# Kernel tuning notes

Measured on AMD Instinct MI355X. Metric: run time of the kernel, lower is better.

The kernel has to match this reference:

```python
import jax, jax.numpy as jnp
import numpy as np

B, S, P, J = 32, 128, 2, 17
DIN, DOUT, DRNN, DHID = 2, 3, 128, 256
N = P * J
DT = 0.1   # delta_t from init
K = 4      # Euler steps, hardcoded k=int(4) in source


def setup_inputs() -> dict:
    key = jax.random.key(0)
    ks = jax.random.split(key, 12)
    g = lambda k, sh, fan: (jax.random.normal(k, sh, jnp.float32) / np.sqrt(fan)).astype(jnp.float32)
    d = {}
    d['x2d'] = jax.random.normal(ks[0], (B, S, P, J, DIN), jnp.float32)
    d['mask'] = jax.random.randint(ks[1], (B, S, P, J, 1), 0, 2).astype(jnp.int32)
    # ODE MLP: DRNN -> DHID -> DHID -> DRNN (num_hidden=2 hidden layers, tanh)
    d['ode_w0'] = g(ks[2], (DRNN, DHID), DRNN); d['ode_b0'] = jnp.zeros((DHID,), jnp.float32)
    d['ode_w1'] = g(ks[3], (DHID, DHID), DHID); d['ode_b1'] = jnp.zeros((DHID,), jnp.float32)
    d['ode_w2'] = g(ks[4], (DHID, DRNN), DHID); d['ode_b2'] = jnp.zeros((DRNN,), jnp.float32)
    # GRU cell 0: input DIN -> hidden DRNN ; GRU cell 1: input DRNN -> hidden DRNN
    d['wih0'] = g(ks[5], (DIN, 3 * DRNN), DIN);  d['whh0'] = g(ks[6], (DRNN, 3 * DRNN), DRNN)
    d['bih0'] = jnp.zeros((3 * DRNN,), jnp.float32); d['bhh0'] = jnp.zeros((3 * DRNN,), jnp.float32)
    d['wih1'] = g(ks[7], (DRNN, 3 * DRNN), DRNN); d['whh1'] = g(ks[8], (DRNN, 3 * DRNN), DRNN)
    d['bih1'] = jnp.zeros((3 * DRNN,), jnp.float32); d['bhh1'] = jnp.zeros((3 * DRNN,), jnp.float32)
    d['wout'] = g(ks[9], (DRNN, DOUT), DRNN); d['bout'] = jnp.zeros((DOUT,), jnp.float32)
    d['h0'] = 0.01 * jax.random.normal(ks[10], (1, 1, DRNN), jnp.float32)
    return d


def _ode(h, w0, b0, w1, b1, w2, b2):
    h = jnp.tanh(h @ w0 + b0)
    h = jnp.tanh(h @ w1 + b1)
    return h @ w2 + b2


def _gru(x, h, wih, whh, bih, bhh):
    gi = x @ wih + bih
    gh = h @ whh + bhh
    ir, iz, ig = jnp.split(gi, 3, axis=-1)
    hr, hz, hg = jnp.split(gh, 3, axis=-1)
    r = jax.nn.sigmoid(ir + hr)
    z = jax.nn.sigmoid(iz + hz)
    n = jnp.tanh(ig + r * hg)
    return (1.0 - z) * n + z * h


def reference(x2d, mask, ode_w0, ode_b0, ode_w1, ode_b1, ode_w2, ode_b2,
              wih0, whh0, bih0, bhh0, wih1, whh1, bih1, bhh1, wout, bout, h0):
    m = mask.astype(x2d.dtype)                      # (B,S,P,J,1)
    xs = (x2d * m).reshape(B, S, N, DIN)            # masked 2D input
    ms = m.reshape(B, S, N, 1)
    h_init = jnp.broadcast_to(h0, (B, N, DRNN))

    def step(h, inp):
        x, mm = inp                                 # (B,N,DIN), (B,N,1)
        h1 = h
        for _ in range(K):                          # 4 Euler ODE steps
            h1 = h1 + DT * _ode(h1, ode_w0, ode_b0, ode_w1, ode_b1, ode_w2, ode_b2)
        h2 = _gru(x, h1, wih0, whh0, bih0, bhh0)    # stacked GRU, both conditioned on h1
        h2 = _gru(h2, h1, wih1, whh1, bih1, bhh1)
        h_next = h1 * (1.0 - mm) + h2 * mm
        return h_next, h1

    _, hs = jax.lax.scan(step, h_init,
                         (jnp.swapaxes(xs, 0, 1), jnp.swapaxes(ms, 0, 1)))
    hs = jnp.swapaxes(hs, 0, 1)                     # (B,S,N,DRNN)
    ys = (hs @ wout + bout).reshape(B, S, P, J, DOUT)
    return ys
```

## Files before the change

### kernel.cpp

```cpp
#include <hip/hip_runtime.h>

typedef _Float16 f16x8 __attribute__((ext_vector_type(8)));
typedef float f32x4 __attribute__((ext_vector_type(4)));

constexpr int S_ = 128;
constexpr float DT_ = 0.1f;
constexpr float LS = 2048.0f;
constexpr float INV = 1.0f / 2048.0f;

#define MFMA(a, b, c) __builtin_amdgcn_mfma_f32_16x16x32_f16((a), (b), (c), 0, 0, 0)

#define OB0   0
#define OB1   256
#define OB2   512
#define OBHH0 640
#define OBIH0 1024
#define OBIH1 1408
#define OBHH1 1792
#define NBIAS 2176

__device__ __forceinline__ float fast_tanh(float x) {
    float e = __expf(2.0f * x);
    return 1.0f - 2.0f / (e + 1.0f);
}
__device__ __forceinline__ float fast_sigmoid(float x) {
    return 1.0f / (1.0f + __expf(-x));
}

__global__ void prep_hl(const float* __restrict__ src, _Float16* __restrict__ hi,
                        _Float16* __restrict__ lo, int K, int N) {
    int e = blockIdx.x * 256 + threadIdx.x;
    if (e >= K * N) return;
    int tile = e >> 9, r = e & 511;
    int lane = r >> 3, j = r & 7;
    int KT = K >> 5;
    int nt = tile / KT, kt = tile - nt * KT;
    int k = kt * 32 + ((lane >> 4) << 3) + j;
    int n = nt * 16 + (lane & 15);
    float v = src[k * N + n];
    _Float16 h = (_Float16)v;
    hi[e] = h;
    lo[e] = (_Float16)((v - (float)h) * LS);
}

__global__ __launch_bounds__(512) void odernn_mfma(
    const float* __restrict__ x2d, const int* __restrict__ maskp,
    const _Float16* __restrict__ w0h, const _Float16* __restrict__ w0l,
    const _Float16* __restrict__ w1hg, const _Float16* __restrict__ w1lg,
    const _Float16* __restrict__ w2h, const _Float16* __restrict__ w2l,
    const _Float16* __restrict__ hh0h, const _Float16* __restrict__ hh0l,
    const _Float16* __restrict__ ih1h, const _Float16* __restrict__ ih1l,
    const _Float16* __restrict__ hh1h, const _Float16* __restrict__ hh1l,
    const float* __restrict__ b0, const float* __restrict__ b1,
    const float* __restrict__ b2, const float* __restrict__ bhh0,
    const float* __restrict__ bih0, const float* __restrict__ wih0,
    const float* __restrict__ bih1, const float* __restrict__ bhh1,
    const float* __restrict__ wout, const float* __restrict__ bout,
    const float* __restrict__ h0, float* __restrict__ out)
{
    __shared__ float hF[16][128];
    __shared__ _Float16 bAh[16][264], bAl[16][264];
    __shared__ _Float16 bBh[16][264], bBl[16][264];
    __shared__ _Float16 bHh[16][136], bHl[16][136];
    __shared__ float sbias[NBIAS];
    __shared__ float swi0[768];
    __shared__ float swout[384];
    __shared__ float sbout[4];
    __shared__ float sx0[16], sx1[16], smm[16];
    __shared__ int sIdx[16];

    const int tid = (int)threadIdx.x;
    const int wv = tid >> 6;
    const int l = tid & 63;
    const int lrow = l & 15;
    const int lk8 = (l >> 4) << 3;
    const int rbase = (l >> 4) << 2;

    for (int e = tid; e < 256; e += 512) { sbias[OB0 + e] = b0[e]; sbias[OB1 + e] = b1[e]; }
    for (int e = tid; e < 128; e += 512) sbias[OB2 + e] = b2[e];
    for (int e = tid; e < 384; e += 512) {
        sbias[OBHH0 + e] = bhh0[e];
        sbias[OBIH0 + e] = bih0[e];
        sbias[OBIH1 + e] = bih1[e];
        sbias[OBHH1 + e] = bhh1[e];
        swout[e] = wout[e];
    }
    for (int e = tid; e < 768; e += 512) swi0[e] = wih0[e];
    if (tid < 3) sbout[tid] = bout[tid];
    for (int e = tid; e < 2048; e += 512) {
        int row = e >> 7, col = e & 127;
        float v = h0[col];
        hF[row][col] = v;
        _Float16 hh = (_Float16)v;
        bHh[row][col] = hh;
        bHl[row][col] = (_Float16)((v - (float)hh) * LS);
    }
    if (tid < 16) {
        int grow = (int)blockIdx.x * 16 + tid;
        int bb = grow / 34, nn = grow - bb * 34;
        sIdx[tid] = bb * (S_ * 34) + nn;
    }
    __syncthreads();

    for (int s = 0; s < S_; ++s) {
        if (tid < 16) {
            int idx = sIdx[tid] + s * 34;
            float fm = (float)maskp[idx];
            smm[tid] = fm;
            sx0[tid] = x2d[2 * idx] * fm;
            sx1[tid] = x2d[2 * idx + 1] * fm;
        }

        for (int it = 0; it < 4; ++it) {
            {
                const int n0 = wv << 4, n1 = (wv + 8) << 4;
                const f16x8* B0h = (const f16x8*)w0h + (size_t)(wv * 4) * 64 + l;
                const f16x8* B0l = (const f16x8*)w0l + (size_t)(wv * 4) * 64 + l;
                const f16x8* B1h = (const f16x8*)w0h + (size_t)((wv + 8) * 4) * 64 + l;
                const f16x8* B1l = (const f16x8*)w0l + (size_t)((wv + 8) * 4) * 64 + l;
                f16x8 bh0[4], bl0[4], bh1[4], bl1[4];
#pragma unroll
                for (int kt = 0; kt < 4; ++kt) {
                    bh0[kt] = B0h[kt * 64]; bl0[kt] = B0l[kt * 64];
                    bh1[kt] = B1h[kt * 64]; bl1[kt] = B1l[kt * 64];
                }
                float bv0 = sbias[OB0 + n0 + lrow], bv1 = sbias[OB0 + n1 + lrow];
                f32x4 a0 = {bv0, bv0, bv0, bv0}, a1 = {bv1, bv1, bv1, bv1};
                f32x4 p0 = {0, 0, 0, 0}, q0 = {0, 0, 0, 0}, p1 = {0, 0, 0, 0}, q1 = {0, 0, 0, 0};
#pragma unroll
                for (int kt = 0; kt < 4; ++kt) {
                    f16x8 ah = *(const f16x8*)&bHh[lrow][kt * 32 + lk8];
                    f16x8 al = *(const f16x8*)&bHl[lrow][kt * 32 + lk8];
                    a0 = MFMA(ah, bh0[kt], a0);
                    p0 = MFMA(ah, bl0[kt], p0);
                    q0 = MFMA(al, bh0[kt], q0);
                    a1 = MFMA(ah, bh1[kt], a1);
                    p1 = MFMA(ah, bl1[kt], p1);
                    q1 = MFMA(al, bh1[kt], q1);
                }
#pragma unroll
                for (int r = 0; r < 4; ++r) {
                    int row = rbase + r;
                    float v0 = fast_tanh(a0[r] + (p0[r] + q0[r]) * INV);
                    float v1 = fast_tanh(a1[r] + (p1[r] + q1[r]) * INV);
                    _Float16 hh = (_Float16)v0;
                    bBh[row][n0 + lrow] = hh;
                    bBl[row][n0 + lrow] = (_Float16)((v0 - (float)hh) * LS);
                    hh = (_Float16)v1;
                    bBh[row][n1 + lrow] = hh;
                    bBl[row][n1 + lrow] = (_Float16)((v1 - (float)hh) * LS);
                }
            }
            __syncthreads();

            {
                const int n0 = wv << 4, n1 = (wv + 8) << 4;
                const f16x8* B0h = (const f16x8*)w1hg + (size_t)(wv * 8) * 64 + l;
                const f16x8* B0l = (const f16x8*)w1lg + (size_t)(wv * 8) * 64 + l;
                const f16x8* B1h = (const f16x8*)w1hg + (size_t)((wv + 8) * 8) * 64 + l;
                const f16x8* B1l = (const f16x8*)w1lg + (size_t)((wv + 8) * 8) * 64 + l;
                f16x8 bh0[8], bl0[8], bh1[8], bl1[8];
#pragma unroll
                for (int kt = 0; kt < 8; ++kt) {
                    bh0[kt] = B0h[kt * 64]; bl0[kt] = B0l[kt * 64];
                    bh1[kt] = B1h[kt * 64]; bl1[kt] = B1l[kt * 64];
                }
                float bv0 = sbias[OB1 + n0 + lrow], bv1 = sbias[OB1 + n1 + lrow];
                f32x4 a0 = {bv0, bv0, bv0, bv0}, a1 = {bv1, bv1, bv1, bv1};
                f32x4 p0 = {0, 0, 0, 0}, q0 = {0, 0, 0, 0}, p1 = {0, 0, 0, 0}, q1 = {0, 0, 0, 0};
#pragma unroll
                for (int kt = 0; kt < 8; ++kt) {
                    f16x8 ah = *(const f16x8*)&bBh[lrow][kt * 32 + lk8];
                    f16x8 al = *(const f16x8*)&bBl[lrow][kt * 32 + lk8];
                    a0 = MFMA(ah, bh0[kt], a0);
                    p0 = MFMA(ah, bl0[kt], p0);
                    q0 = MFMA(al, bh0[kt], q0);
                    a1 = MFMA(ah, bh1[kt], a1);
                    p1 = MFMA(ah, bl1[kt], p1);
                    q1 = MFMA(al, bh1[kt], q1);
                }
#pragma unroll
                for (int r = 0; r < 4; ++r) {
                    int row = rbase + r;
                    float v0 = fast_tanh(a0[r] + (p0[r] + q0[r]) * INV);
                    float v1 = fast_tanh(a1[r] + (p1[r] + q1[r]) * INV);
                    _Float16 hh = (_Float16)v0;
                    bAh[row][n0 + lrow] = hh;
                    bAl[row][n0 + lrow] = (_Float16)((v0 - (float)hh) * LS);
                    hh = (_Float16)v1;
                    bAh[row][n1 + lrow] = hh;
                    bAl[row][n1 + lrow] = (_Float16)((v1 - (float)hh) * LS);
                }
            }
            __syncthreads();

            {
                const int n0 = wv << 4;
                const f16x8* Bh = (const f16x8*)w2h + (size_t)(wv * 8) * 64 + l;
                const f16x8* Bl = (const f16x8*)w2l + (size_t)(wv * 8) * 64 + l;
                f16x8 bh[8], bl[8];
#pragma unroll
                for (int kt = 0; kt < 8; ++kt) { bh[kt] = Bh[kt * 64]; bl[kt] = Bl[kt * 64]; }
                float bv = sbias[OB2 + n0 + lrow];
                f32x4 acc = {bv, bv, bv, bv};
                f32x4 pp = {0, 0, 0, 0}, qq = {0, 0, 0, 0};
#pragma unroll
                for (int kt = 0; kt < 8; ++kt) {
                    f16x8 ah = *(const f16x8*)&bAh[lrow][kt * 32 + lk8];
                    f16x8 al = *(const f16x8*)&bAl[lrow][kt * 32 + lk8];
                    acc = MFMA(ah, bh[kt], acc);
                    pp = MFMA(ah, bl[kt], pp);
                    qq = MFMA(al, bh[kt], qq);
                }
#pragma unroll
                for (int r = 0; r < 4; ++r) {
                    int row = rbase + r, col = n0 + lrow;
                    float v = hF[row][col] + DT_ * (acc[r] + (pp[r] + qq[r]) * INV);
                    hF[row][col] = v;
                    _Float16 hh = (_Float16)v;
                    bHh[row][col] = hh;
                    bHl[row][col] = (_Float16)((v - (float)hh) * LS);
                }
            }
            __syncthreads();
        }

        {
            f16x8 bh[3][4], bl[3][4];
#pragma unroll
            for (int t = 0; t < 3; ++t) {
                const f16x8* Bh = (const f16x8*)hh0h + (size_t)((wv + (t << 3)) * 4) * 64 + l;
                const f16x8* Bl = (const f16x8*)hh0l + (size_t)((wv + (t << 3)) * 4) * 64 + l;
#pragma unroll
                for (int kt = 0; kt < 4; ++kt) { bh[t][kt] = Bh[kt * 64]; bl[t][kt] = Bl[kt * 64]; }
            }
            f32x4 acc0, acc1, acc2;
            f32x4 p0 = {0,0,0,0}, q0 = {0,0,0,0}, p1 = {0,0,0,0}, q1 = {0,0,0,0}, p2 = {0,0,0,0}, q2 = {0,0,0,0};
            {
                float v0 = sbias[OBHH0 + ((wv) << 4) + lrow];
                float v1 = sbias[OBHH0 + ((wv + 8) << 4) + lrow];
                float v2 = sbias[OBHH0 + ((wv + 16) << 4) + lrow];
                acc0 = (f32x4){v0, v0, v0, v0};
                acc1 = (f32x4){v1, v1, v1, v1};
                acc2 = (f32x4){v2, v2, v2, v2};
            }
#pragma unroll
            for (int kt = 0; kt < 4; ++kt) {
                f16x8 ah = *(const f16x8*)&bHh[lrow][kt * 32 + lk8];
                f16x8 al = *(const f16x8*)&bHl[lrow][kt * 32 + lk8];
                acc0 = MFMA(ah, bh[0][kt], acc0); p0 = MFMA(ah, bl[0][kt], p0); q0 = MFMA(al, bh[0][kt], q0);
                acc1 = MFMA(ah, bh[1][kt], acc1); p1 = MFMA(ah, bl[1][kt], p1); q1 = MFMA(al, bh[1][kt], q1);
                acc2 = MFMA(ah, bh[2][kt], acc2); p2 = MFMA(ah, bl[2][kt], p2); q2 = MFMA(al, bh[2][kt], q2);
            }
            {
                int yrow = wv + ((l >> 5) << 3);
                int ll = l & 31;
                int c0 = ll << 2;
                float4 hv = *(const float4*)&hF[yrow][c0];
                float y0 = hv.x * swout[c0 * 3] + hv.y * swout[(c0 + 1) * 3] +
                           hv.z * swout[(c0 + 2) * 3] + hv.w * swout[(c0 + 3) * 3];
                float y1 = hv.x * swout[c0 * 3 + 1] + hv.y * swout[(c0 + 1) * 3 + 1] +
                           hv.z * swout[(c0 + 2) * 3 + 1] + hv.w * swout[(c0 + 3) * 3 + 1];
                float y2 = hv.x * swout[c0 * 3 + 2] + hv.y * swout[(c0 + 1) * 3 + 2] +
                           hv.z * swout[(c0 + 2) * 3 + 2] + hv.w * swout[(c0 + 3) * 3 + 2];
#pragma unroll
                for (int m = 16; m >= 1; m >>= 1) {
                    y0 += __shfl_xor(y0, m, 64);
                    y1 += __shfl_xor(y1, m, 64);
                    y2 += __shfl_xor(y2, m, 64);
                }
                if (ll == 0) {
                    int idx = sIdx[yrow] + s * 34;
                    out[idx * 3 + 0] = y0 + sbout[0];
                    out[idx * 3 + 1] = y1 + sbout[1];
                    out[idx * 3 + 2] = y2 + sbout[2];
                }
            }
            {
                int col = (wv << 4) + lrow;
                float wxr0 = swi0[col], wxr1 = swi0[384 + col];
                float wxz0 = swi0[128 + col], wxz1 = swi0[384 + 128 + col];
                float wxn0 = swi0[256 + col], wxn1 = swi0[384 + 256 + col];
                float bir = sbias[OBIH0 + col], biz = sbias[OBIH0 + 128 + col], bin = sbias[OBIH0 + 256 + col];
#pragma unroll
                for (int r = 0; r < 4; ++r) {
                    int row = rbase + r;
                    float ghr = acc0[r] + (p0[r] + q0[r]) * INV;
                    float ghz = acc1[r] + (p1[r] + q1[r]) * INV;
                    float ghn = acc2[r] + (p2[r] + q2[r]) * INV;
                    float xa = sx0[row], xb = sx1[row];
                    float rg = fast_sigmoid(bir + xa * wxr0 + xb * wxr1 + ghr);
                    float zg = fast_sigmoid(biz + xa * wxz0 + xb * wxz1 + ghz);
                    float nn = fast_tanh(bin + xa * wxn0 + xb * wxn1 + rg * ghn);
                    float h1 = hF[row][col];
                    float h2 = (1.0f - zg) * nn + zg * h1;
                    _Float16 hh = (_Float16)h2;
                    bBh[row][col] = hh;
                    bBl[row][col] = (_Float16)((h2 - (float)hh) * LS);
                }
            }
        }
        __syncthreads();

        {
            f32x4 gi0, gi1, gi2;
            {
                f16x8 bh[3][4], bl[3][4];
#pragma unroll
                for (int t = 0; t < 3; ++t) {
                    const f16x8* Bh = (const f16x8*)ih1h + (size_t)((wv + (t << 3)) * 4) * 64 + l;
                    const f16x8* Bl = (const f16x8*)ih1l + (size_t)((wv + (t << 3)) * 4) * 64 + l;
#pragma unroll
                    for (int kt = 0; kt < 4; ++kt) { bh[t][kt] = Bh[kt * 64]; bl[t][kt] = Bl[kt * 64]; }
                }
                f32x4 a0, a1, a2;
                f32x4 p0 = {0,0,0,0}, q0 = {0,0,0,0}, p1 = {0,0,0,0}, q1 = {0,0,0,0}, p2 = {0,0,0,0}, q2 = {0,0,0,0};
                {
                    float v0 = sbias[OBIH1 + ((wv) << 4) + lrow];
                    float v1 = sbias[OBIH1 + ((wv + 8) << 4) + lrow];
                    float v2 = sbias[OBIH1 + ((wv + 16) << 4) + lrow];
                    a0 = (f32x4){v0, v0, v0, v0};
                    a1 = (f32x4){v1, v1, v1, v1};
                    a2 = (f32x4){v2, v2, v2, v2};
                }
#pragma unroll
                for (int kt = 0; kt < 4; ++kt) {
                    f16x8 ah = *(const f16x8*)&bBh[lrow][kt * 32 + lk8];
                    f16x8 al = *(const f16x8*)&bBl[lrow][kt * 32 + lk8];
                    a0 = MFMA(ah, bh[0][kt], a0); p0 = MFMA(ah, bl[0][kt], p0); q0 = MFMA(al, bh[0][kt], q0);
                    a1 = MFMA(ah, bh[1][kt], a1); p1 = MFMA(ah, bl[1][kt], p1); q1 = MFMA(al, bh[1][kt], q1);
                    a2 = MFMA(ah, bh[2][kt], a2); p2 = MFMA(ah, bl[2][kt], p2); q2 = MFMA(al, bh[2][kt], q2);
                }
                gi0 = a0 + (p0 + q0) * INV;
                gi1 = a1 + (p1 + q1) * INV;
                gi2 = a2 + (p2 + q2) * INV;
            }

            f32x4 aH0, aH1, aH2;
            f32x4 pH0 = {0,0,0,0}, qH0 = {0,0,0,0}, pH1 = {0,0,0,0}, qH1 = {0,0,0,0}, pH2 = {0,0,0,0}, qH2 = {0,0,0,0};
            {
                f16x8 bh[3][4], bl[3][4];
#pragma unroll
                for (int t = 0; t < 3; ++t) {
                    const f16x8* Bh = (const f16x8*)hh1h + (size_t)((wv + (t << 3)) * 4) * 64 + l;
                    const f16x8* Bl = (const f16x8*)hh1l + (size_t)((wv + (t << 3)) * 4) * 64 + l;
#pragma unroll
                    for (int kt = 0; kt < 4; ++kt) { bh[t][kt] = Bh[kt * 64]; bl[t][kt] = Bl[kt * 64]; }
                }
                {
                    float v0 = sbias[OBHH1 + ((wv) << 4) + lrow];
                    float v1 = sbias[OBHH1 + ((wv + 8) << 4) + lrow];
                    float v2 = sbias[OBHH1 + ((wv + 16) << 4) + lrow];
                    aH0 = (f32x4){v0, v0, v0, v0};
                    aH1 = (f32x4){v1, v1, v1, v1};
                    aH2 = (f32x4){v2, v2, v2, v2};
                }
#pragma unroll
                for (int kt = 0; kt < 4; ++kt) {
                    f16x8 ah = *(const f16x8*)&bHh[lrow][kt * 32 + lk8];
                    f16x8 al = *(const f16x8*)&bHl[lrow][kt * 32 + lk8];
                    aH0 = MFMA(ah, bh[0][kt], aH0); pH0 = MFMA(ah, bl[0][kt], pH0); qH0 = MFMA(al, bh[0][kt], qH0);
                    aH1 = MFMA(ah, bh[1][kt], aH1); pH1 = MFMA(ah, bl[1][kt], pH1); qH1 = MFMA(al, bh[1][kt], qH1);
                    aH2 = MFMA(ah, bh[2][kt], aH2); pH2 = MFMA(ah, bl[2][kt], pH2); qH2 = MFMA(al, bh[2][kt], qH2);
                }
            }
            __syncthreads();
#pragma unroll
            for (int r = 0; r < 4; ++r) {
                int row = rbase + r, col = (wv << 4) + lrow;
                float ghr = aH0[r] + (pH0[r] + qH0[r]) * INV;
                float ghz = aH1[r] + (pH1[r] + qH1[r]) * INV;
                float ghn = aH2[r] + (pH2[r] + qH2[r]) * INV;
                float rg = fast_sigmoid(gi0[r] + ghr);
                float zg = fast_sigmoid(gi1[r] + ghz);
                float nn = fast_tanh(gi2[r] + rg * ghn);
                float h1 = hF[row][col];
                float h2 = (1.0f - zg) * nn + zg * h1;
                float v = (smm[row] != 0.0f) ? h2 : h1;
                hF[row][col] = v;
                _Float16 hh = (_Float16)v;
                bHh[row][col] = hh;
                bHl[row][col] = (_Float16)((v - (float)hh) * LS);
            }
        }
        __syncthreads();
    }
}

extern "C" void kernel_launch(void* const* d_in, const int* in_sizes, int n_in,
                              void* d_out, int out_size, void* d_ws, size_t ws_size,
                              hipStream_t stream) {
    const float* x2d  = (const float*)d_in[0];
    const int*   mask = (const int*)d_in[1];
    const float* w0   = (const float*)d_in[2];
    const float* b0   = (const float*)d_in[3];
    const float* w1   = (const float*)d_in[4];
    const float* b1   = (const float*)d_in[5];
    const float* w2   = (const float*)d_in[6];
    const float* b2   = (const float*)d_in[7];
    const float* wih0 = (const float*)d_in[8];
    const float* whh0 = (const float*)d_in[9];
    const float* bih0 = (const float*)d_in[10];
    const float* bhh0 = (const float*)d_in[11];
    const float* wih1 = (const float*)d_in[12];
    const float* whh1 = (const float*)d_in[13];
    const float* bih1 = (const float*)d_in[14];
    const float* bhh1 = (const float*)d_in[15];
    const float* wout = (const float*)d_in[16];
    const float* bout = (const float*)d_in[17];
    const float* h0   = (const float*)d_in[18];
    float* out = (float*)d_out;

    _Float16* base = (_Float16*)d_ws;
    _Float16* pw0h  = base;
    _Float16* pw1h  = base + 32768;
    _Float16* pw2h  = base + 98304;
    _Float16* ph0h  = base + 131072;
    _Float16* pi1h  = base + 180224;
    _Float16* ph1h  = base + 229376;
    _Float16* lobase = base + 278528;
    _Float16* pw0l  = lobase;
    _Float16* pw1l  = lobase + 32768;
    _Float16* pw2l  = lobase + 98304;
    _Float16* ph0l  = lobase + 131072;
    _Float16* pi1l  = lobase + 180224;
    _Float16* ph1l  = lobase + 229376;

    hipLaunchKernelGGL(prep_hl, dim3(128), dim3(256), 0, stream, w0,   pw0h, pw0l, 128, 256);
    hipLaunchKernelGGL(prep_hl, dim3(256), dim3(256), 0, stream, w1,   pw1h, pw1l, 256, 256);
    hipLaunchKernelGGL(prep_hl, dim3(128), dim3(256), 0, stream, w2,   pw2h, pw2l, 256, 128);
    hipLaunchKernelGGL(prep_hl, dim3(192), dim3(256), 0, stream, whh0, ph0h, ph0l, 128, 384);
    hipLaunchKernelGGL(prep_hl, dim3(192), dim3(256), 0, stream, wih1, pi1h, pi1l, 128, 384);
    hipLaunchKernelGGL(prep_hl, dim3(192), dim3(256), 0, stream, whh1, ph1h, ph1l, 128, 384);

    hipLaunchKernelGGL(odernn_mfma, dim3(68), dim3(512), 0, stream,
        x2d, mask, pw0h, pw0l, pw1h, pw1l, pw2h, pw2l,
        ph0h, ph0l, pi1h, pi1l, ph1h, ph1l,
        b0, b1, b2, bhh0, bih0, wih0, bih1, bhh1, wout, bout, h0, out);
}
```

Before: 7.343 ms.

## Drop weight prep kernels and split fp32 weights into fp16 hi/lo inside the recurrent kernel

Removes the six prep_hl launches that pre-split the weights into packed fp16 hi/lo tiles. The main kernel now loads the raw fp32 weights with strided scalar reads and converts them to hi/lo fragments on the fly before each MFMA. This saves the prep launches and workspace traffic, but each step now reads twice the bytes with uncoalesced strided loads and repeats the conversion arithmetic, inside a 128-step by 4-iteration loop. It also adds a launch_bounds hint of 2 blocks per CU.

```diff
diff --git a/kernel.cpp b/kernel.cpp
--- a/kernel.cpp
+++ b/kernel.cpp
@@ -27,33 +27,45 @@
     return 1.0f / (1.0f + __expf(-x));
 }
 
-__global__ void prep_hl(const float* __restrict__ src, _Float16* __restrict__ hi,
-                        _Float16* __restrict__ lo, int K, int N) {
-    int e = blockIdx.x * 256 + threadIdx.x;
-    if (e >= K * N) return;
-    int tile = e >> 9, r = e & 511;
-    int lane = r >> 3, j = r & 7;
-    int KT = K >> 5;
-    int nt = tile / KT, kt = tile - nt * KT;
-    int k = kt * 32 + ((lane >> 4) << 3) + j;
-    int n = nt * 16 + (lane & 15);
-    float v = src[k * N + n];
-    _Float16 h = (_Float16)v;
-    hi[e] = h;
-    lo[e] = (_Float16)((v - (float)h) * LS);
-}
-
-__global__ __launch_bounds__(512) void odernn_mfma(
+template<int KT>
+__device__ __forceinline__ void wtile_mm(
+    const float* __restrict__ W, int N, int nt,
+    const _Float16* __restrict__ Ah, const _Float16* __restrict__ Al, int lda,
+    int lrow, int lk8, f32x4& acc, f32x4& pe, f32x4& qe)
+{
+    const float* base = W + (size_t)lk8 * N + nt * 16 + lrow;
+    float raw[KT][8];
+#pragma unroll
+    for (int kt = 0; kt < KT; ++kt)
+#pragma unroll
+        for (int j = 0; j < 8; ++j)
+            raw[kt][j] = base[(kt * 32 + j) * (size_t)N];
+#pragma unroll
+    for (int kt = 0; kt < KT; ++kt) {
+        f16x8 bh, bl;
+#pragma unroll
+        for (int j = 0; j < 8; ++j) {
+            float v = raw[kt][j];
+            _Float16 h = (_Float16)v;
+            bh[j] = h;
+            bl[j] = (_Float16)((v - (float)h) * LS);
+        }
+        f16x8 ah = *(const f16x8*)(Ah + lrow * lda + kt * 32 + lk8);
+        f16x8 al = *(const f16x8*)(Al + lrow * lda + kt * 32 + lk8);
+        acc = MFMA(ah, bh, acc);
+        pe  = MFMA(ah, bl, pe);
+        qe  = MFMA(al, bh, qe);
+    }
+}
+
+__global__ __launch_bounds__(512, 2) void odernn_mfma(
     const float* __restrict__ x2d, const int* __restrict__ maskp,
-    const _Float16* __restrict__ w0h, const _Float16* __restrict__ w0l,
-    const _Float16* __restrict__ w1hg, const _Float16* __restrict__ w1lg,
-    const _Float16* __restrict__ w2h, const _Float16* __restrict__ w2l,
-    const _Float16* __restrict__ hh0h, const _Float16* __restrict__ hh0l,
-    const _Float16* __restrict__ ih1h, const _Float16* __restrict__ ih1l,
-    const _Float16* __restrict__ hh1h, const _Float16* __restrict__ hh1l,
-    const float* __restrict__ b0, const float* __restrict__ b1,
-    const float* __restrict__ b2, const float* __restrict__ bhh0,
-    const float* __restrict__ bih0, const float* __restrict__ wih0,
+    const float* __restrict__ w0, const float* __restrict__ b0,
+    const float* __restrict__ w1, const float* __restrict__ b1,
+    const float* __restrict__ w2, const float* __restrict__ b2,
+    const float* __restrict__ wih0, const float* __restrict__ whh0,
+    const float* __restrict__ bih0, const float* __restrict__ bhh0,
+    const float* __restrict__ wih1, const float* __restrict__ whh1,
     const float* __restrict__ bih1, const float* __restrict__ bhh1,
     const float* __restrict__ wout, const float* __restrict__ bout,
     const float* __restrict__ h0, float* __restrict__ out)
@@ -114,30 +126,11 @@
         for (int it = 0; it < 4; ++it) {
             {
                 const int n0 = wv << 4, n1 = (wv + 8) << 4;
-                const f16x8* B0h = (const f16x8*)w0h + (size_t)(wv * 4) * 64 + l;
-                const f16x8* B0l = (const f16x8*)w0l + (size_t)(wv * 4) * 64 + l;
-                const f16x8* B1h = (const f16x8*)w0h + (size_t)((wv + 8) * 4) * 64 + l;
-                const f16x8* B1l = (const f16x8*)w0l + (size_t)((wv + 8) * 4) * 64 + l;
-                f16x8 bh0[4], bl0[4], bh1[4], bl1[4];
-#pragma unroll
-                for (int kt = 0; kt < 4; ++kt) {
-                    bh0[kt] = B0h[kt * 64]; bl0[kt] = B0l[kt * 64];
-                    bh1[kt] = B1h[kt * 64]; bl1[kt] = B1l[kt * 64];
-                }
                 float bv0 = sbias[OB0 + n0 + lrow], bv1 = sbias[OB0 + n1 + lrow];
                 f32x4 a0 = {bv0, bv0, bv0, bv0}, a1 = {bv1, bv1, bv1, bv1};
                 f32x4 p0 = {0, 0, 0, 0}, q0 = {0, 0, 0, 0}, p1 = {0, 0, 0, 0}, q1 = {0, 0, 0, 0};
-#pragma unroll
-                for (int kt = 0; kt < 4; ++kt) {
-                    f16x8 ah = *(const f16x8*)&bHh[lrow][kt * 32 + lk8];
-                    f16x8 al = *(const f16x8*)&bHl[lrow][kt * 32 + lk8];
-                    a0 = MFMA(ah, bh0[kt], a0);
-                    p0 = MFMA(ah, bl0[kt], p0);
-                    q0 = MFMA(al, bh0[kt], q0);
-                    a1 = MFMA(ah, bh1[kt], a1);
-                    p1 = MFMA(ah, bl1[kt], p1);
-                    q1 = MFMA(al, bh1[kt], q1);
-                }
+                wtile_mm<4>(w0, 256, wv,     &bHh[0][0], &bHl[0][0], 136, lrow, lk8, a0, p0, q0);
+                wtile_mm<4>(w0, 256, wv + 8, &bHh[0][0], &bHl[0][0], 136, lrow, lk8, a1, p1, q1);
 #pragma unroll
                 for (int r = 0; r < 4; ++r) {
                     int row = rbase + r;
@@ -155,30 +148,11 @@
 
             {
                 const int n0 = wv << 4, n1 = (wv + 8) << 4;
-                const f16x8* B0h = (const f16x8*)w1hg + (size_t)(wv * 8) * 64 + l;
-                const f16x8* B0l = (const f16x8*)w1lg + (size_t)(wv * 8) * 64 + l;
-                const f16x8* B1h = (const f16x8*)w1hg + (size_t)((wv + 8) * 8) * 64 + l;
-                const f16x8* B1l = (const f16x8*)w1lg + (size_t)((wv + 8) * 8) * 64 + l;
-                f16x8 bh0[8], bl0[8], bh1[8], bl1[8];
-#pragma unroll
-                for (int kt = 0; kt < 8; ++kt) {
-                    bh0[kt] = B0h[kt * 64]; bl0[kt] = B0l[kt * 64];
-                    bh1[kt] = B1h[kt * 64]; bl1[kt] = B1l[kt * 64];
-                }
                 float bv0 = sbias[OB1 + n0 + lrow], bv1 = sbias[OB1 + n1 + lrow];
                 f32x4 a0 = {bv0, bv0, bv0, bv0}, a1 = {bv1, bv1, bv1, bv1};
                 f32x4 p0 = {0, 0, 0, 0}, q0 = {0, 0, 0, 0}, p1 = {0, 0, 0, 0}, q1 = {0, 0, 0, 0};
-#pragma unroll
-                for (int kt = 0; kt < 8; ++kt) {
-                    f16x8 ah = *(const f16x8*)&bBh[lrow][kt * 32 + lk8];
-                    f16x8 al = *(const f16x8*)&bBl[lrow][kt * 32 + lk8];
-                    a0 = MFMA(ah, bh0[kt], a0);
-                    p0 = MFMA(ah, bl0[kt], p0);
-                    q0 = MFMA(al, bh0[kt], q0);
-                    a1 = MFMA(ah, bh1[kt], a1);
-                    p1 = MFMA(ah, bl1[kt], p1);
-                    q1 = MFMA(al, bh1[kt], q1);
-                }
+                wtile_mm<8>(w1, 256, wv,     &bBh[0][0], &bBl[0][0], 264, lrow, lk8, a0, p0, q0);
+                wtile_mm<8>(w1, 256, wv + 8, &bBh[0][0], &bBl[0][0], 264, lrow, lk8, a1, p1, q1);
 #pragma unroll
                 for (int r = 0; r < 4; ++r) {
                     int row = rbase + r;
@@ -196,22 +170,10 @@
 
             {
                 const int n0 = wv << 4;
-                const f16x8* Bh = (const f16x8*)w2h + (size_t)(wv * 8) * 64 + l;
-                const f16x8* Bl = (const f16x8*)w2l + (size_t)(wv * 8) * 64 + l;
-                f16x8 bh[8], bl[8];
-#pragma unroll
-                for (int kt = 0; kt < 8; ++kt) { bh[kt] = Bh[kt * 64]; bl[kt] = Bl[kt * 64]; }
                 float bv = sbias[OB2 + n0 + lrow];
                 f32x4 acc = {bv, bv, bv, bv};
                 f32x4 pp = {0, 0, 0, 0}, qq = {0, 0, 0, 0};
-#pragma unroll
-                for (int kt = 0; kt < 8; ++kt) {
-                    f16x8 ah = *(const f16x8*)&bAh[lrow][kt * 32 + lk8];
-                    f16x8 al = *(const f16x8*)&bAl[lrow][kt * 32 + lk8];
-                    acc = MFMA(ah, bh[kt], acc);
-                    pp = MFMA(ah, bl[kt], pp);
-                    qq = MFMA(al, bh[kt], qq);
-                }
+                wtile_mm<8>(w2, 128, wv, &bAh[0][0], &bAl[0][0], 264, lrow, lk8, acc, pp, qq);
 #pragma unroll
                 for (int r = 0; r < 4; ++r) {
                     int row = rbase + r, col = n0 + lrow;
@@ -226,14 +188,6 @@
         }
 
         {
-            f16x8 bh[3][4], bl[3][4];
-#pragma unroll
-            for (int t = 0; t < 3; ++t) {
-                const f16x8* Bh = (const f16x8*)hh0h + (size_t)((wv + (t << 3)) * 4) * 64 + l;
-                const f16x8* Bl = (const f16x8*)hh0l + (size_t)((wv + (t << 3)) * 4) * 64 + l;
-#pragma unroll
-                for (int kt = 0; kt < 4; ++kt) { bh[t][kt] = Bh[kt * 64]; bl[t][kt] = Bl[kt * 64]; }
-            }
             f32x4 acc0, acc1, acc2;
             f32x4 p0 = {0,0,0,0}, q0 = {0,0,0,0}, p1 = {0,0,0,0}, q1 = {0,0,0,0}, p2 = {0,0,0,0}, q2 = {0,0,0,0};
             {
@@ -244,14 +198,9 @@
                 acc1 = (f32x4){v1, v1, v1, v1};
                 acc2 = (f32x4){v2, v2, v2, v2};
             }
-#pragma unroll
-            for (int kt = 0; kt < 4; ++kt) {
-                f16x8 ah = *(const f16x8*)&bHh[lrow][kt * 32 + lk8];
-                f16x8 al = *(const f16x8*)&bHl[lrow][kt * 32 + lk8];
-                acc0 = MFMA(ah, bh[0][kt], acc0); p0 = MFMA(ah, bl[0][kt], p0); q0 = MFMA(al, bh[0][kt], q0);
-                acc1 = MFMA(ah, bh[1][kt], acc1); p1 = MFMA(ah, bl[1][kt], p1); q1 = MFMA(al, bh[1][kt], q1);
-                acc2 = MFMA(ah, bh[2][kt], acc2); p2 = MFMA(ah, bl[2][kt], p2); q2 = MFMA(al, bh[2][kt], q2);
-            }
+            wtile_mm<4>(whh0, 384, wv,      &bHh[0][0], &bHl[0][0], 136, lrow, lk8, acc0, p0, q0);
+            wtile_mm<4>(whh0, 384, wv + 8,  &bHh[0][0], &bHl[0][0], 136, lrow, lk8, acc1, p1, q1);
+            wtile_mm<4>(whh0, 384, wv + 16, &bHh[0][0], &bHl[0][0], 136, lrow, lk8, acc2, p2, q2);
             {
                 int yrow = wv + ((l >> 5) << 3);
                 int ll = l & 31;
@@ -305,14 +254,6 @@
         {
             f32x4 gi0, gi1, gi2;
             {
-                f16x8 bh[3][4], bl[3][4];
-#pragma unroll
-                for (int t = 0; t < 3; ++t) {
-                    const f16x8* Bh = (const f16x8*)ih1h + (size_t)((wv + (t << 3)) * 4) * 64 + l;
-                    const f16x8* Bl = (const f16x8*)ih1l + (size_t)((wv + (t << 3)) * 4) * 64 + l;
-#pragma unroll
-                    for (int kt = 0; kt < 4; ++kt) { bh[t][kt] = Bh[kt * 64]; bl[t][kt] = Bl[kt * 64]; }
-                }
                 f32x4 a0, a1, a2;
                 f32x4 p0 = {0,0,0,0}, q0 = {0,0,0,0}, p1 = {0,0,0,0}, q1 = {0,0,0,0}, p2 = {0,0,0,0}, q2 = {0,0,0,0};
                 {
@@ -323,14 +264,9 @@
                     a1 = (f32x4){v1, v1, v1, v1};
                     a2 = (f32x4){v2, v2, v2, v2};
                 }
-#pragma unroll
-                for (int kt = 0; kt < 4; ++kt) {
-                    f16x8 ah = *(const f16x8*)&bBh[lrow][kt * 32 + lk8];
-                    f16x8 al = *(const f16x8*)&bBl[lrow][kt * 32 + lk8];
-                    a0 = MFMA(ah, bh[0][kt], a0); p0 = MFMA(ah, bl[0][kt], p0); q0 = MFMA(al, bh[0][kt], q0);
-                    a1 = MFMA(ah, bh[1][kt], a1); p1 = MFMA(ah, bl[1][kt], p1); q1 = MFMA(al, bh[1][kt], q1);
-                    a2 = MFMA(ah, bh[2][kt], a2); p2 = MFMA(ah, bl[2][kt], p2); q2 = MFMA(al, bh[2][kt], q2);
-                }
+                wtile_mm<4>(wih1, 384, wv,      &bBh[0][0], &bBl[0][0], 264, lrow, lk8, a0, p0, q0);
+                wtile_mm<4>(wih1, 384, wv + 8,  &bBh[0][0], &bBl[0][0], 264, lrow, lk8, a1, p1, q1);
+                wtile_mm<4>(wih1, 384, wv + 16, &bBh[0][0], &bBl[0][0], 264, lrow, lk8, a2, p2, q2);
                 gi0 = a0 + (p0 + q0) * INV;
                 gi1 = a1 + (p1 + q1) * INV;
                 gi2 = a2 + (p2 + q2) * INV;
@@ -339,31 +275,17 @@
             f32x4 aH0, aH1, aH2;
             f32x4 pH0 = {0,0,0,0}, qH0 = {0,0,0,0}, pH1 = {0,0,0,0}, qH1 = {0,0,0,0}, pH2 = {0,0,0,0}, qH2 = {0,0,0,0};
             {
-                f16x8 bh[3][4], bl[3][4];
-#pragma unroll
-                for (int t = 0; t < 3; ++t) {
-                    const f16x8* Bh = (const f16x8*)hh1h + (size_t)((wv + (t << 3)) * 4) * 64 + l;
-                    const f16x8* Bl = (const f16x8*)hh1l + (size_t)((wv + (t << 3)) * 4) * 64 + l;
-#pragma unroll
-                    for (int kt = 0; kt < 4; ++kt) { bh[t][kt] = Bh[kt * 64]; bl[t][kt] = Bl[kt * 64]; }
-                }
-                {
-                    float v0 = sbias[OBHH1 + ((wv) << 4) + lrow];
-                    float v1 = sbias[OBHH1 + ((wv + 8) << 4) + lrow];
-                    float v2 = sbias[OBHH1 + ((wv + 16) << 4) + lrow];
-                    aH0 = (f32x4){v0, v0, v0, v0};
-                    aH1 = (f32x4){v1, v1, v1, v1};
-                    aH2 = (f32x4){v2, v2, v2, v2};
-                }
-#pragma unroll
-                for (int kt = 0; kt < 4; ++kt) {
-                    f16x8 ah = *(const f16x8*)&bHh[lrow][kt * 32 + lk8];
-                    f16x8 al = *(const f16x8*)&bHl[lrow][kt * 32 + lk8];
-                    aH0 = MFMA(ah, bh[0][kt], aH0); pH0 = MFMA(ah, bl[0][kt], pH0); qH0 = MFMA(al, bh[0][kt], qH0);
-                    aH1 = MFMA(ah, bh[1][kt], aH1); pH1 = MFMA(ah, bl[1][kt], pH1); qH1 = MFMA(al, bh[1][kt], qH1);
-                    aH2 = MFMA(ah, bh[2][kt], aH2); pH2 = MFMA(ah, bl[2][kt], pH2); qH2 = MFMA(al, bh[2][kt], qH2);
-                }
-            }
+                float v0 = sbias[OBHH1 + ((wv) << 4) + lrow];
+                float v1 = sbias[OBHH1 + ((wv + 8) << 4) + lrow];
+                float v2 = sbias[OBHH1 + ((wv + 16) << 4) + lrow];
+                aH0 = (f32x4){v0, v0, v0, v0};
+                aH1 = (f32x4){v1, v1, v1, v1};
+                aH2 = (f32x4){v2, v2, v2, v2};
+            }
+            wtile_mm<4>(whh1, 384, wv,      &bHh[0][0], &bHl[0][0], 136, lrow, lk8, aH0, pH0, qH0);
+            wtile_mm<4>(whh1, 384, wv + 8,  &bHh[0][0], &bHl[0][0], 136, lrow, lk8, aH1, pH1, qH1);
+            wtile_mm<4>(whh1, 384, wv + 16, &bHh[0][0], &bHl[0][0], 136, lrow, lk8, aH2, pH2, qH2);
+
             __syncthreads();
 #pragma unroll
             for (int r = 0; r < 4; ++r) {
@@ -411,30 +333,8 @@
     const float* h0   = (const float*)d_in[18];
     float* out = (float*)d_out;
 
-    _Float16* base = (_Float16*)d_ws;
-    _Float16* pw0h  = base;
-    _Float16* pw1h  = base + 32768;
-    _Float16* pw2h  = base + 98304;
-    _Float16* ph0h  = base + 131072;
-    _Float16* pi1h  = base + 180224;
-    _Float16* ph1h  = base + 229376;
-    _Float16* lobase = base + 278528;
-    _Float16* pw0l  = lobase;
-    _Float16* pw1l  = lobase + 32768;
-    _Float16* pw2l  = lobase + 98304;
-    _Float16* ph0l  = lobase + 131072;
-    _Float16* pi1l  = lobase + 180224;
-    _Float16* ph1l  = lobase + 229376;
-
-    hipLaunchKernelGGL(prep_hl, dim3(128), dim3(256), 0, stream, w0,   pw0h, pw0l, 128, 256);
-    hipLaunchKernelGGL(prep_hl, dim3(256), dim3(256), 0, stream, w1,   pw1h, pw1l, 256, 256);
-    hipLaunchKernelGGL(prep_hl, dim3(128), dim3(256), 0, stream, w2,   pw2h, pw2l, 256, 128);
-    hipLaunchKernelGGL(prep_hl, dim3(192), dim3(256), 0, stream, whh0, ph0h, ph0l, 128, 384);
-    hipLaunchKernelGGL(prep_hl, dim3(192), dim3(256), 0, stream, wih1, pi1h, pi1l, 128, 384);
-    hipLaunchKernelGGL(prep_hl, dim3(192), dim3(256), 0, stream, whh1, ph1h, ph1l, 128, 384);
-
     hipLaunchKernelGGL(odernn_mfma, dim3(68), dim3(512), 0, stream,
-        x2d, mask, pw0h, pw0l, pw1h, pw1l, pw2h, pw2l,
-        ph0h, ph0l, pi1h, pi1l, ph1h, ph1l,
-        b0, b1, b2, bhh0, bih0, wih0, bih1, bhh1, wout, bout, h0, out);
-}
+        x2d, mask, w0, b0, w1, b1, w2, b2,
+        wih0, whh0, bih0, bhh0, wih1, whh1, bih1, bhh1,
+        wout, bout, h0, out);
+}
```

Result: no change. 7.217 ms (-1.7%).
